# Kernel optimization log

Measured on AMD Instinct MI355X. Metric: run time of the kernel, lower is better.

The kernel has to match this reference:

```python
import jax, jax.numpy as jnp
import numpy as np

B, S, D = 2, 2048, 2048
H, KVH, HD = 16, 4, 128
E, TOPK, FF = 8, 2, 4096
EPS = 1e-6
THETA = 1000000.0


def setup_inputs() -> dict:
    key = jax.random.key(0)
    ks = jax.random.split(key, 12)
    s = 0.02
    return {
        'hidden_states': jax.random.normal(ks[0], (B, S, D), jnp.float32),
        'attention_mask': jnp.ones((B, S), dtype=bool),
        'wq': jax.random.normal(ks[1], (D, H * HD), jnp.float32) * s,
        'wk': jax.random.normal(ks[2], (D, KVH * HD), jnp.float32) * s,
        'wv': jax.random.normal(ks[3], (D, KVH * HD), jnp.float32) * s,
        'wo': jax.random.normal(ks[4], (H * HD, D), jnp.float32) * s,
        'ln1_w': jnp.ones((D,), jnp.float32),
        'ln2_w': jnp.ones((D,), jnp.float32),
        'gate_w': jax.random.normal(ks[5], (D, E), jnp.float32) * s,
        'w_gate': jax.random.normal(ks[6], (E, D, FF), jnp.float32) * s,
        'w_up': jax.random.normal(ks[7], (E, D, FF), jnp.float32) * s,
        'w_down': jax.random.normal(ks[8], (E, FF, D), jnp.float32) * s,
    }


def rms_norm(x, w):
    xf = x.astype(jnp.float32)
    var = jnp.mean(jnp.square(xf), axis=-1, keepdims=True)
    return w * (xf * jax.lax.rsqrt(var + EPS)).astype(x.dtype)


def rotate_half(x):
    x1, x2 = x[..., : x.shape[-1] // 2], x[..., x.shape[-1] // 2 :]
    return jnp.concatenate((-x2, x1), axis=-1)


def attention(x, mask, wq, wk, wv, wo):
    q = (x @ wq).reshape(B, S, H, HD)
    k = (x @ wk).reshape(B, S, KVH, HD)
    v = (x @ wv).reshape(B, S, KVH, HD)
    # RoPE (fp32 freqs, as in MixtralRotaryEmbedding)
    inv_freq = 1.0 / (THETA ** (jnp.arange(0, HD, 2, dtype=jnp.float32) / HD))
    freqs = jnp.arange(S, dtype=jnp.float32)[:, None] * inv_freq[None, :]  # [S, HD/2]
    emb = jnp.concatenate([freqs, freqs], axis=-1)  # [S, HD]
    cos = jnp.cos(emb)[None, :, None, :]  # [1,S,1,HD]
    sin = jnp.sin(emb)[None, :, None, :]
    q = q * cos + rotate_half(q) * sin
    k = k * cos + rotate_half(k) * sin
    # GQA: repeat kv heads
    k = jnp.repeat(k, H // KVH, axis=2)
    v = jnp.repeat(v, H // KVH, axis=2)
    # faithful to source: keep-mask is triu(ones, k=1) (strictly-above-diagonal)
    causal = jnp.triu(jnp.ones((S, S), dtype=bool), k=1)
    combined = mask[:, None, None, :] & causal[None, None, :, :]  # [B,1,S,S]
    neg = jnp.finfo(jnp.float32).min
    bias = jnp.where(combined, 0.0, neg).astype(jnp.float32)
    scores = jnp.einsum('bqhd,bkhd->bhqk', q, k) * (HD ** -0.5) + bias
    attn = jax.nn.softmax(scores, axis=-1)
    out = jnp.einsum('bhqk,bkhd->bqhd', attn, v).reshape(B, S, H * HD)
    return out @ wo


def moe(x, gate_w, w_gate, w_up, w_down):
    # x: [T, D]
    T = x.shape[0]
    logits = x.astype(jnp.float32) @ gate_w  # fp32 router, [T, E]
    rw = jax.nn.softmax(logits, axis=-1)
    top_w, top_i = jax.lax.top_k(rw, TOPK)
    top_w = top_w / jnp.sum(top_w, axis=-1, keepdims=True)
    w_full = jnp.zeros((T, E), jnp.float32).at[jnp.arange(T)[:, None], top_i].set(top_w)
    out = jnp.zeros_like(x)
    for e in range(E):  # small fixed expert loop
        h = jax.nn.silu(x @ w_gate[e]) * (x @ w_up[e])
        out = out + w_full[:, e, None] * (h @ w_down[e])
    return out


def reference(hidden_states, attention_mask, wq, wk, wv, wo, ln1_w, ln2_w, gate_w, w_gate, w_up, w_down):
    residual = hidden_states
    h = rms_norm(hidden_states, ln1_w)
    h = residual + attention(h, attention_mask, wq, wk, wv, wo)
    residual = h
    h = rms_norm(h, ln2_w)
    m = moe(h.reshape(-1, D), gate_w, w_gate, w_up, w_down).reshape(B, S, D)
    return residual + m
```

## Files before the change

kernel.cpp:

```cpp
#include <hip/hip_runtime.h>
#include <cstdint>
#include <cstddef>


typedef unsigned short u16;
typedef __attribute__((ext_vector_type(8))) short short8;
typedef __attribute__((ext_vector_type(8))) _Float16 half8;
typedef __attribute__((ext_vector_type(8))) __bf16 bf16x8;
typedef __attribute__((ext_vector_type(4))) float f32x4;
typedef __attribute__((ext_vector_type(4))) u16 us4;
typedef __attribute__((ext_vector_type(4))) unsigned int u32x4;

__device__ __forceinline__ u16 f2bf(float f) {
  unsigned u = __builtin_bit_cast(unsigned, f);
  u += 0x7fffu + ((u >> 16) & 1u);
  return (u16)(u >> 16);
}
__device__ __forceinline__ void splitf16(float x, float scale, u16 &hi, u16 &lo) {
  float xs = x * scale;
  _Float16 h = (_Float16)xs;
  hi = __builtin_bit_cast(u16, h);
  _Float16 l = (_Float16)(xs - (float)h);
  lo = __builtin_bit_cast(u16, l);
}
__device__ __forceinline__ f32x4 mma_bf(short8 a, short8 b, f32x4 c) {
  return __builtin_amdgcn_mfma_f32_16x16x32_bf16(
      __builtin_bit_cast(bf16x8, a), __builtin_bit_cast(bf16x8, b), c, 0, 0, 0);
}
__device__ __forceinline__ f32x4 mma_h(short8 a, short8 b, f32x4 c) {
  return __builtin_amdgcn_mfma_f32_16x16x32_f16(
      __builtin_bit_cast(half8, a), __builtin_bit_cast(half8, b), c, 0, 0, 0);
}
__device__ __forceinline__ void gl16(const u16 *g, u16 *l) {
  __builtin_amdgcn_global_load_lds(
      (const __attribute__((address_space(1))) unsigned *)g,
      (__attribute__((address_space(3))) unsigned *)l, 16, 0, 0);
}

template <int OM>
__global__ __launch_bounds__(256) void k_trans(
    const float *__restrict__ src, u16 *__restrict__ d0, u16 *__restrict__ d1,
    int ld_src, int ld_dst, long long zhi, long long zlo, int zmod,
    long long dstz, int inter, float scale) {
  int z = blockIdx.z;
  src += (long long)(z / zmod) * zhi + (long long)(z % zmod) * zlo;
  d0 += (long long)z * dstz;
  if constexpr (OM == 1) d1 += (long long)z * dstz;
  int r0 = blockIdx.y * 64, c0 = blockIdx.x * 64;
  __shared__ float t[64][65];
  int tx = threadIdx.x;
  int rr = tx >> 4, cc = (tx & 15) * 4;
#pragma unroll
  for (int i = 0; i < 4; i++) {
    float4 v = *(const float4 *)(src + (size_t)(r0 + rr + i * 16) * ld_src + c0 + cc);
    t[rr + i * 16][cc] = v.x; t[rr + i * 16][cc + 1] = v.y;
    t[rr + i * 16][cc + 2] = v.z; t[rr + i * 16][cc + 3] = v.w;
  }
  __syncthreads();
#pragma unroll
  for (int i = 0; i < 4; i++) {
    int c = rr + i * 16;
    int f = c0 + c;
    int drow = (inter < 0) ? f : (((f >> 5) << 6) + (f & 31) + (inter << 5));
    size_t bo = (size_t)drow * ld_dst + r0 + cc;
    if constexpr (OM == 0) {
      us4 o;
#pragma unroll
      for (int j = 0; j < 4; j++) o[j] = f2bf(t[cc + j][c]);
      *(us4 *)(d0 + bo) = o;
    } else {
      us4 oh, ol;
#pragma unroll
      for (int j = 0; j < 4; j++) {
        u16 a, b; splitf16(t[cc + j][c], scale, a, b);
        oh[j] = a; ol[j] = b;
      }
      *(us4 *)(d0 + bo) = oh;
      *(us4 *)(d1 + bo) = ol;
    }
  }
}

__global__ __launch_bounds__(256) void k_rms(
    const float *__restrict__ x, const float *__restrict__ w,
    u16 *__restrict__ oh, u16 *__restrict__ ol, float scale16) {
  int row = blockIdx.x, tid = threadIdx.x;
  const float *xr = x + (size_t)row * 2048;
  float4 v0 = *(const float4 *)(xr + tid * 8);
  float4 v1 = *(const float4 *)(xr + tid * 8 + 4);
  float ss = v0.x * v0.x + v0.y * v0.y + v0.z * v0.z + v0.w * v0.w +
             v1.x * v1.x + v1.y * v1.y + v1.z * v1.z + v1.w * v1.w;
  __shared__ float red[256];
  red[tid] = ss;
  __syncthreads();
  for (int s = 128; s > 0; s >>= 1) {
    if (tid < s) red[tid] += red[tid + s];
    __syncthreads();
  }
  float sc = rsqrtf(red[0] * (1.0f / 2048.0f) + 1e-6f);
  float4 w0 = *(const float4 *)(w + tid * 8);
  float4 w1 = *(const float4 *)(w + tid * 8 + 4);
  float o[8] = {v0.x * sc * w0.x, v0.y * sc * w0.y, v0.z * sc * w0.z, v0.w * sc * w0.w,
                v1.x * sc * w1.x, v1.y * sc * w1.y, v1.z * sc * w1.z, v1.w * sc * w1.w};
  size_t bo = (size_t)row * 2048 + tid * 8;
  if (ol) {
    us4 h0, h1, l0, l1;
#pragma unroll
    for (int j = 0; j < 4; j++) {
      u16 a, b;
      splitf16(o[j], scale16, a, b); h0[j] = a; l0[j] = b;
      splitf16(o[j + 4], scale16, a, b); h1[j] = a; l1[j] = b;
    }
    *(us4 *)(oh + bo) = h0; *(us4 *)(oh + bo + 4) = h1;
    *(us4 *)(ol + bo) = l0; *(us4 *)(ol + bo + 4) = l1;
  } else {
    us4 a, b;
#pragma unroll
    for (int j = 0; j < 4; j++) { a[j] = f2bf(o[j]); b[j] = f2bf(o[j + 4]); }
    *(us4 *)(oh + bo) = a; *(us4 *)(oh + bo + 4) = b;
  }
}

__global__ void k_cs(float2 *__restrict__ cs) {
  int idx = blockIdx.x * 256 + threadIdx.x;
  int s = idx >> 6, i = idx & 63;
  double inv = exp2(-(double)i * (19.931568569324174 / 64.0));
  double ang = (double)s * inv;
  cs[idx] = make_float2((float)cos(ang), (float)sin(ang));
}

__global__ __launch_bounds__(256) void k_rope(
    const float *__restrict__ qkv, const float2 *__restrict__ cs,
    u16 *__restrict__ qh, u16 *__restrict__ ql,
    u16 *__restrict__ kh, u16 *__restrict__ kl) {
  int t = blockIdx.x, tid = threadIdx.x;
  int s = t & 2047;
  const float *bp = qkv + (size_t)t * 3072;
  for (int p = tid; p < 1024; p += 256) {
    int hh = p >> 6, i = p & 63;
    float2 c = cs[s * 64 + i];
    float x1 = bp[hh * 128 + i], x2 = bp[hh * 128 + 64 + i];
    float o1 = x1 * c.x - x2 * c.y, o2 = x2 * c.x + x1 * c.y;
    size_t b1 = (size_t)t * 2048 + hh * 128 + i;
    u16 a, b;
    splitf16(o1, 16.f, a, b); qh[b1] = a; ql[b1] = b;
    splitf16(o2, 16.f, a, b); qh[b1 + 64] = a; ql[b1 + 64] = b;
  }
  {
    int hh = tid >> 6, i = tid & 63;
    float2 c = cs[s * 64 + i];
    float x1 = bp[2048 + hh * 128 + i], x2 = bp[2048 + hh * 128 + 64 + i];
    float o1 = x1 * c.x - x2 * c.y, o2 = x2 * c.x + x1 * c.y;
    size_t b1 = (size_t)t * 512 + hh * 128 + i;
    u16 a, b;
    splitf16(o1, 16.f, a, b); kh[b1] = a; kl[b1] = b;
    splitf16(o2, 16.f, a, b); kh[b1 + 64] = a; kl[b1 + 64] = b;
  }
}

__global__ __launch_bounds__(256) void k_attn(
    const u16 *__restrict__ qh, const u16 *__restrict__ ql,
    const u16 *__restrict__ kh, const u16 *__restrict__ kl,
    const u16 *__restrict__ vh, const u16 *__restrict__ vl,
    u16 *__restrict__ oh, u16 *__restrict__ ol) {
  const int qt = blockIdx.x, kvh = blockIdx.y, b = blockIdx.z;
  const int q0 = qt * 16;
  const int tid = threadIdx.x, wid = tid >> 6, lane = tid & 63;
  const int h = kvh * 4 + wid;
  const int lr = lane & 15, g = lane >> 4, lk = g * 8;
  const float SC = 0.08838834764831845f * 1.44269504088896341f / 256.0f;

  __shared__ alignas(16) u16 KT[2][2][4096];
  __shared__ alignas(16) u16 VT[2][2][4096];
  __shared__ alignas(16) u16 Pb[4][2][512];

  short8 qfh[4], qfl[4];
  {
    size_t qo = (size_t)(b * 2048 + q0 + lr) * 2048 + h * 128 + lk;
#pragma unroll
    for (int c = 0; c < 4; c++) {
      qfh[c] = *(const short8 *)(qh + qo + c * 32);
      qfl[c] = *(const short8 *)(ql + qo + c * 32);
    }
  }
  f32x4 accO[8] = {};
  float m_r[4], l_r[4];
#pragma unroll
  for (int r = 0; r < 4; r++) { m_r[r] = -3.0e38f; l_r[r] = 0.f; }

  const int kv_start = (q0 == 2032) ? 0 : (((q0 + 1) >> 5) << 5);
  const int nIter = (2048 - kv_start) >> 5;

  const u16 *khp = kh + (size_t)(b * 2048) * 512 + kvh * 128;
  const u16 *klp = kl + (size_t)(b * 2048) * 512 + kvh * 128;
  const u16 *vhp = vh + ((size_t)(b * 4 + kvh) * 128) * 2048;
  const u16 *vlp = vl + ((size_t)(b * 4 + kvh) * 128) * 2048;

  auto stage = [&](int bf, int kv0) {
#pragma unroll
    for (int j = 0; j < 2; j++) {
      const int c0 = wid * 128 + j * 64;
      const int cc = c0 + lane;
      const int krow = cc >> 4, kcol = (cc & 15) ^ (krow & 7);
      const size_t kg = (size_t)(kv0 + krow) * 512 + kcol * 8;
      gl16(khp + kg, &KT[bf][0][c0 * 8]);
      gl16(klp + kg, &KT[bf][1][c0 * 8]);
      const int vd = cc >> 2, vi = (cc & 3) ^ (vd & 3);
      const size_t vg = (size_t)vd * 2048 + kv0 + vi * 8;
      gl16(vhp + vg, &VT[bf][0][c0 * 8]);
      gl16(vlp + vg, &VT[bf][1][c0 * 8]);
    }
  };

  stage(0, kv_start);
  __syncthreads();
  int buf = 0;
  for (int it = 0; it < nIter; it++) {
    const int kv0 = kv_start + (it << 5);
    if (it + 1 < nIter) stage(buf ^ 1, kv0 + 32);
    f32x4 s0 = {}, s1 = {};
    {
      const u16 *KhL = KT[buf][0], *KlL = KT[buf][1];
#pragma unroll
      for (int c = 0; c < 4; c++) {
        const int idx0 = lr * 128 + (((c * 4 + g) ^ (lr & 7)) << 3);
        const int idx1 = idx0 + 2048;
        short8 k0h = *(const short8 *)(KhL + idx0);
        short8 k0l = *(const short8 *)(KlL + idx0);
        short8 k1h = *(const short8 *)(KhL + idx1);
        short8 k1l = *(const short8 *)(KlL + idx1);
        s0 = mma_h(qfh[c], k0h, s0); s0 = mma_h(qfh[c], k0l, s0); s0 = mma_h(qfl[c], k0h, s0);
        s1 = mma_h(qfh[c], k1h, s1); s1 = mma_h(qfh[c], k1l, s1); s1 = mma_h(qfl[c], k1h, s1);
      }
    }
    const bool msk = (kv0 <= q0 + 15);
    float alpha[4];
#pragma unroll
    for (int r = 0; r < 4; r++) {
      float v0 = s0[r] * SC, v1 = s1[r] * SC;
      if (msk) {
        int rowq = q0 + g * 4 + r;
        if (kv0 + lr <= rowq) v0 = -3.0e38f;
        if (kv0 + 16 + lr <= rowq) v1 = -3.0e38f;
      }
      float mx = fmaxf(v0, v1);
#pragma unroll
      for (int o = 1; o < 16; o <<= 1) mx = fmaxf(mx, __shfl_xor(mx, o));
      float mn = fmaxf(m_r[r], mx);
      float p0 = exp2f(v0 - mn), p1 = exp2f(v1 - mn);
      float sum = p0 + p1;
#pragma unroll
      for (int o = 1; o < 16; o <<= 1) sum += __shfl_xor(sum, o);
      alpha[r] = exp2f(m_r[r] - mn);
      l_r[r] = l_r[r] * alpha[r] + sum;
      m_r[r] = mn;
      const int prow = g * 4 + r;
      const int sc0 = lr | (((0 ^ g) & 3) << 3) + 0;
      (void)sc0;
      {
        int c0l = lr, c1l = 16 + lr;
        int p0i = prow * 32 + ((c0l & 7) | ((((c0l >> 3) ^ g) & 3) << 3));
        int p1i = prow * 32 + ((c1l & 7) | ((((c1l >> 3) ^ g) & 3) << 3));
        u16 x, y;
        splitf16(p0, 16.f, x, y); Pb[wid][0][p0i] = x; Pb[wid][1][p0i] = y;
        splitf16(p1, 16.f, x, y); Pb[wid][0][p1i] = x; Pb[wid][1][p1i] = y;
      }
    }
#pragma unroll
    for (int nt = 0; nt < 8; nt++) {
      f32x4 t = accO[nt];
      t[0] *= alpha[0]; t[1] *= alpha[1]; t[2] *= alpha[2]; t[3] *= alpha[3];
      accO[nt] = t;
    }
    asm volatile("s_waitcnt lgkmcnt(0)" ::: "memory");
    const int pidx = lr * 32 + (((g ^ (lr >> 2)) & 3) << 3);
    short8 pfh = *(const short8 *)(&Pb[wid][0][pidx]);
    short8 pfl = *(const short8 *)(&Pb[wid][1][pidx]);
    {
      const u16 *VhL = VT[buf][0], *VlL = VT[buf][1];
#pragma unroll
      for (int nt = 0; nt < 8; nt++) {
        const int d = nt * 16 + lr;
        const int vidx = d * 32 + (((g ^ (d & 3)) & 3) << 3);
        short8 wfh = *(const short8 *)(VhL + vidx);
        short8 wfl = *(const short8 *)(VlL + vidx);
        f32x4 t = accO[nt];
        t = mma_h(pfh, wfh, t); t = mma_h(pfh, wfl, t); t = mma_h(pfl, wfh, t);
        accO[nt] = t;
      }
    }
    __syncthreads();
    buf ^= 1;
  }
  float inv[4];
#pragma unroll
  for (int r = 0; r < 4; r++) inv[r] = 1.0f / (l_r[r] * 256.0f);
#pragma unroll
  for (int nt = 0; nt < 8; nt++)
#pragma unroll
    for (int r = 0; r < 4; r++) {
      float v = accO[nt][r] * inv[r];
      size_t idx = (size_t)(b * 2048 + q0 + g * 4 + r) * 2048 + h * 128 + nt * 16 + lr;
      u16 x, y; splitf16(v, 16.f, x, y);
      oh[idx] = x; ol[idx] = y;
    }
}

template <int MODE>
__global__ __launch_bounds__(256) void k_gemm(
    const u16 *__restrict__ Ah, const u16 *__restrict__ Al,
    const u16 *__restrict__ Bh, const u16 *__restrict__ Bl,
    int M, int N, int K, int lda, int ldb, int ldc, float descale,
    float *__restrict__ outf, const float *__restrict__ resid,
    u16 *__restrict__ outh,
    const int *__restrict__ offs, const int *__restrict__ counts,
    const int *__restrict__ row_token, const float *__restrict__ row_w) {
  constexpr bool SPLIT = (MODE <= 1);
  const int tid = threadIdx.x;
  const int wid = tid >> 6, lane = tid & 63;
  const int wr = wid >> 1, wc = wid & 1;
  const int l15 = lane & 15, l4 = lane >> 4;
  const int n0 = blockIdx.x * 128, m0 = blockIdx.y * 128;
  int seg = 0, cnt = M;
  if constexpr (MODE >= 2) {
    int e = blockIdx.z;
    seg = offs[e]; cnt = counts[e];
    if (m0 >= cnt) return;
    Bh += (size_t)e * (size_t)N * (size_t)ldb;
  }
  __shared__ alignas(16) u16 AsH[4096], BsH[4096];
  __shared__ alignas(16) u16 AsL[SPLIT ? 4096 : 8], BsL[SPLIT ? 4096 : 8];
  const int r16 = lane >> 2, c8 = (lane & 3) << 3;
  int a0 = m0 + wid * 16 + r16, a1 = a0 + 64;
  if constexpr (MODE >= 2) {
    if (a0 > cnt - 1) a0 = cnt - 1;
    if (a1 > cnt - 1) a1 = cnt - 1;
  }
  const u16 *pa0 = Ah + (size_t)(seg + a0) * lda + c8;
  const u16 *pa1 = Ah + (size_t)(seg + a1) * lda + c8;
  const int b0 = n0 + wid * 16 + r16, b1 = b0 + 64;
  const u16 *pb0 = Bh + (size_t)b0 * ldb + c8;
  const u16 *pb1 = Bh + (size_t)b1 * ldb + c8;
  const u16 *qa0 = nullptr, *qa1 = nullptr, *qb0 = nullptr, *qb1 = nullptr;
  if constexpr (SPLIT) {
    qa0 = Al + (size_t)a0 * lda + c8;
    qa1 = Al + (size_t)a1 * lda + c8;
    qb0 = Bl + (size_t)b0 * ldb + c8;
    qb1 = Bl + (size_t)b1 * ldb + c8;
  }
  u16 *sa0 = AsH + wid * 512, *sa1 = AsH + 2048 + wid * 512;
  u16 *sb0 = BsH + wid * 512, *sb1 = BsH + 2048 + wid * 512;
  f32x4 acc[4][4] = {};
  const int fa = (wr * 64 + l15) * 32 + (l4 << 3);
  const int fb = (wc * 64 + l15) * 32 + (l4 << 3);
  for (int k0 = 0; k0 < K; k0 += 32) {
    gl16(pa0 + k0, sa0); gl16(pa1 + k0, sa1);
    gl16(pb0 + k0, sb0); gl16(pb1 + k0, sb1);
    if constexpr (SPLIT) {
      gl16(qa0 + k0, AsL + wid * 512); gl16(qa1 + k0, AsL + 2048 + wid * 512);
      gl16(qb0 + k0, BsL + wid * 512); gl16(qb1 + k0, BsL + 2048 + wid * 512);
    }
    __syncthreads();
    short8 ah[4], bh[4];
#pragma unroll
    for (int i = 0; i < 4; i++) ah[i] = *(const short8 *)(AsH + fa + i * 512);
#pragma unroll
    for (int i = 0; i < 4; i++) bh[i] = *(const short8 *)(BsH + fb + i * 512);
    if constexpr (SPLIT) {
      short8 al[4], bl[4];
#pragma unroll
      for (int i = 0; i < 4; i++) al[i] = *(const short8 *)(AsL + fa + i * 512);
#pragma unroll
      for (int i = 0; i < 4; i++) bl[i] = *(const short8 *)(BsL + fb + i * 512);
#pragma unroll
      for (int mi = 0; mi < 4; mi++)
#pragma unroll
        for (int ni = 0; ni < 4; ni++) {
          f32x4 c = acc[mi][ni];
          c = mma_h(ah[mi], bh[ni], c);
          c = mma_h(ah[mi], bl[ni], c);
          c = mma_h(al[mi], bh[ni], c);
          acc[mi][ni] = c;
        }
    } else {
#pragma unroll
      for (int mi = 0; mi < 4; mi++)
#pragma unroll
        for (int ni = 0; ni < 4; ni++)
          acc[mi][ni] = mma_bf(ah[mi], bh[ni], acc[mi][ni]);
    }
    __syncthreads();
  }
  if constexpr (MODE == 0 || MODE == 1) {
#pragma unroll
    for (int mi = 0; mi < 4; mi++)
#pragma unroll
      for (int q = 0; q < 4; q++) {
        int row = m0 + wr * 64 + l4 * 4 + mi * 16 + q;
        size_t rb = (size_t)row * ldc;
#pragma unroll
        for (int ni = 0; ni < 4; ni++) {
          int col = n0 + wc * 64 + ni * 16 + l15;
          float v = acc[mi][ni][q] * descale;
          if constexpr (MODE == 1) v += resid[rb + col];
          outf[rb + col] = v;
        }
      }
  } else if constexpr (MODE == 2) {
    int f0 = (n0 + wc * 64) >> 1;
#pragma unroll
    for (int mi = 0; mi < 4; mi++)
#pragma unroll
      for (int q = 0; q < 4; q++) {
        int rl = m0 + wr * 64 + l4 * 4 + mi * 16 + q;
        if (rl < cnt) {
          size_t rb = (size_t)(seg + rl) * ldc;
#pragma unroll
          for (int nt = 0; nt < 2; nt++) {
            float gg = acc[mi][nt][q], u = acc[mi][nt + 2][q];
            float hv = (gg / (1.0f + __expf(-gg))) * u;
            outh[rb + f0 + nt * 16 + l15] = f2bf(hv);
          }
        }
      }
  } else {
#pragma unroll
    for (int mi = 0; mi < 4; mi++)
#pragma unroll
      for (int q = 0; q < 4; q++) {
        int rl = m0 + wr * 64 + l4 * 4 + mi * 16 + q;
        if (rl < cnt) {
          int tok = row_token[seg + rl];
          float w = row_w[seg + rl];
          size_t rb = (size_t)tok * ldc;
#pragma unroll
          for (int ni = 0; ni < 4; ni++)
            atomicAdd(outf + rb + n0 + wc * 64 + ni * 16 + l15,
                      w * acc[mi][ni][q]);
        }
      }
  }
}

__global__ __launch_bounds__(64) void k_router(
    const float *__restrict__ hb, const float *__restrict__ w2,
    const float *__restrict__ gw, int *__restrict__ topi,
    float *__restrict__ topw, int *__restrict__ counts) {
  const int t = blockIdx.x, lane = threadIdx.x;
  const float *xr = hb + (size_t)t * 2048;
  float xs[32];
  float ss = 0.f;
#pragma unroll
  for (int c = 0; c < 8; c++) {
    float4 v = *(const float4 *)(xr + c * 256 + lane * 4);
    xs[c * 4 + 0] = v.x; xs[c * 4 + 1] = v.y; xs[c * 4 + 2] = v.z; xs[c * 4 + 3] = v.w;
    ss += v.x * v.x + v.y * v.y + v.z * v.z + v.w * v.w;
  }
#pragma unroll
  for (int o = 1; o < 64; o <<= 1) ss += __shfl_xor(ss, o);
  const float sc = rsqrtf(ss * (1.0f / 2048.0f) + 1e-6f);
  float acc[8] = {0, 0, 0, 0, 0, 0, 0, 0};
#pragma unroll
  for (int c = 0; c < 8; c++)
#pragma unroll
    for (int j = 0; j < 4; j++) {
      int d = c * 256 + lane * 4 + j;
      float xn = xs[c * 4 + j] * sc * w2[d];
      float4 g0 = *(const float4 *)(gw + (size_t)d * 8);
      float4 g1 = *(const float4 *)(gw + (size_t)d * 8 + 4);
      acc[0] += xn * g0.x; acc[1] += xn * g0.y; acc[2] += xn * g0.z; acc[3] += xn * g0.w;
      acc[4] += xn * g1.x; acc[5] += xn * g1.y; acc[6] += xn * g1.z; acc[7] += xn * g1.w;
    }
#pragma unroll
  for (int e = 0; e < 8; e++) {
    float v = acc[e];
#pragma unroll
    for (int o = 1; o < 64; o <<= 1) v += __shfl_xor(v, o);
    acc[e] = v;
  }
  if (lane == 0) {
    float mx = acc[0];
#pragma unroll
    for (int e = 1; e < 8; e++) mx = fmaxf(mx, acc[e]);
    float p[8];
#pragma unroll
    for (int e = 0; e < 8; e++) p[e] = __expf(acc[e] - mx);
    int e0 = 0;
#pragma unroll
    for (int e = 1; e < 8; e++) if (p[e] > p[e0]) e0 = e;
    int e1 = (e0 == 0) ? 1 : 0;
#pragma unroll
    for (int e = 0; e < 8; e++) if (e != e0 && p[e] > p[e1]) e1 = e;
    float s2 = p[e0] + p[e1];
    topi[t * 2] = e0; topi[t * 2 + 1] = e1;
    topw[t * 2] = p[e0] / s2; topw[t * 2 + 1] = p[e1] / s2;
    atomicAdd(counts + e0, 1);
    atomicAdd(counts + e1, 1);
  }
}

__global__ void k_zero(int *__restrict__ p) {
  if (threadIdx.x < 8) p[threadIdx.x] = 0;
}
__global__ void k_offsets(const int *__restrict__ counts, int *__restrict__ offs,
                          int *__restrict__ cursors) {
  if (threadIdx.x == 0) {
    int o = 0;
    for (int e = 0; e < 8; e++) { offs[e] = o; o += counts[e]; cursors[e] = 0; }
    offs[8] = o;
  }
}
__global__ __launch_bounds__(256) void k_scatter(
    const int *__restrict__ topi, const float *__restrict__ topw,
    const int *__restrict__ offs, int *__restrict__ cursors,
    int *__restrict__ row_token, float *__restrict__ row_w) {
  int t = blockIdx.x * 256 + threadIdx.x;
  if (t >= 4096) return;
#pragma unroll
  for (int s = 0; s < 2; s++) {
    int e = topi[t * 2 + s];
    int pos = offs[e] + atomicAdd(cursors + e, 1);
    row_token[pos] = t;
    row_w[pos] = topw[t * 2 + s];
  }
}
__global__ __launch_bounds__(256) void k_gather(
    const u16 *__restrict__ h2, const int *__restrict__ row_token,
    u16 *__restrict__ xg) {
  int r = blockIdx.x;
  int t = row_token[r];
  ((u32x4 *)(xg + (size_t)r * 2048))[threadIdx.x] =
      ((const u32x4 *)(h2 + (size_t)t * 2048))[threadIdx.x];
}

extern "C" void kernel_launch(void *const *d_in, const int *in_sizes, int n_in,
                              void *d_out, int out_size, void *d_ws,
                              size_t ws_size, hipStream_t stream) {
  const float *hidden = (const float *)d_in[0];
  const float *wq = (const float *)d_in[2];
  const float *wk = (const float *)d_in[3];
  const float *wv = (const float *)d_in[4];
  const float *wo = (const float *)d_in[5];
  const float *ln1 = (const float *)d_in[6];
  const float *ln2 = (const float *)d_in[7];
  const float *gw = (const float *)d_in[8];
  const float *wg = (const float *)d_in[9];
  const float *wu = (const float *)d_in[10];
  const float *wd = (const float *)d_in[11];
  float *out = (float *)d_out;

  char *base = (char *)d_ws;
  size_t off = 0;
  auto alloc = [&](size_t bytes) -> char * {
    char *p = base + off;
    off += (bytes + 255) & ~(size_t)255;
    return p;
  };
  u16 *wqkvTh = (u16 *)alloc((size_t)3072 * 2048 * 2);
  u16 *wqkvTl = (u16 *)alloc((size_t)3072 * 2048 * 2);
  u16 *woTh = (u16 *)alloc((size_t)2048 * 2048 * 2);
  u16 *woTl = (u16 *)alloc((size_t)2048 * 2048 * 2);
  u16 *wguT = (u16 *)alloc((size_t)8 * 8192 * 2048 * 2);
  u16 *wdT = (u16 *)alloc((size_t)8 * 2048 * 4096 * 2);
  u16 *h1h = (u16 *)alloc((size_t)4096 * 2048 * 2);
  u16 *h1l = (u16 *)alloc((size_t)4096 * 2048 * 2);
  float *qkv = (float *)alloc((size_t)4096 * 3072 * 4);
  u16 *qbh = (u16 *)alloc((size_t)4096 * 2048 * 2);
  u16 *qbl = (u16 *)alloc((size_t)4096 * 2048 * 2);
  u16 *kbh = (u16 *)alloc((size_t)4096 * 512 * 2);
  u16 *kbl = (u16 *)alloc((size_t)4096 * 512 * 2);
  u16 *vth = (u16 *)alloc((size_t)8 * 128 * 2048 * 2);
  u16 *vtl = (u16 *)alloc((size_t)8 * 128 * 2048 * 2);
  float2 *cs = (float2 *)alloc((size_t)2048 * 64 * 8);
  u16 *aoh = (u16 *)alloc((size_t)4096 * 2048 * 2);
  u16 *aol = (u16 *)alloc((size_t)4096 * 2048 * 2);
  u16 *h2 = (u16 *)alloc((size_t)4096 * 2048 * 2);
  int *topi = (int *)alloc(4096 * 2 * 4);
  float *topwt = (float *)alloc(4096 * 2 * 4);
  int *counts = (int *)alloc(64 * 4);
  int *offs = (int *)alloc(64 * 4);
  int *cursors = (int *)alloc(64 * 4);
  int *row_token = (int *)alloc(8192 * 4);
  float *row_w = (float *)alloc(8192 * 4);
  u16 *xg = (u16 *)alloc((size_t)8192 * 2048 * 2);
  u16 *Hb = (u16 *)alloc((size_t)8192 * 4096 * 2);
  if (off > ws_size) return;

  dim3 T256(256), T64(64);
  k_cs<<<dim3(512), T256, 0, stream>>>(cs);
  k_trans<1><<<dim3(32, 32, 1), T256, 0, stream>>>(wq, wqkvTh, wqkvTl, 2048, 2048, 0, 0, 1, 0, -1, 256.f);
  k_trans<1><<<dim3(8, 32, 1), T256, 0, stream>>>(wk, wqkvTh + (size_t)2048 * 2048, wqkvTl + (size_t)2048 * 2048, 512, 2048, 0, 0, 1, 0, -1, 256.f);
  k_trans<1><<<dim3(8, 32, 1), T256, 0, stream>>>(wv, wqkvTh + (size_t)2560 * 2048, wqkvTl + (size_t)2560 * 2048, 512, 2048, 0, 0, 1, 0, -1, 256.f);
  k_trans<1><<<dim3(32, 32, 1), T256, 0, stream>>>(wo, woTh, woTl, 2048, 2048, 0, 0, 1, 0, -1, 256.f);
  k_trans<0><<<dim3(64, 32, 8), T256, 0, stream>>>(wg, wguT, nullptr, 4096, 2048, (long long)2048 * 4096, 0, 1, (long long)8192 * 2048, 0, 1.f);
  k_trans<0><<<dim3(64, 32, 8), T256, 0, stream>>>(wu, wguT, nullptr, 4096, 2048, (long long)2048 * 4096, 0, 1, (long long)8192 * 2048, 1, 1.f);
  k_trans<0><<<dim3(32, 64, 8), T256, 0, stream>>>(wd, wdT, nullptr, 2048, 4096, (long long)4096 * 2048, 0, 1, (long long)2048 * 4096, -1, 1.f);
  k_rms<<<dim3(4096), T256, 0, stream>>>(hidden, ln1, h1h, h1l, 16.f);
  k_gemm<0><<<dim3(24, 32, 1), T256, 0, stream>>>(
      h1h, h1l, wqkvTh, wqkvTl, 4096, 3072, 2048, 2048, 2048, 3072,
      1.f / 4096.f, qkv, nullptr, nullptr, nullptr, nullptr, nullptr, nullptr);
  k_rope<<<dim3(4096), T256, 0, stream>>>(qkv, cs, qbh, qbl, kbh, kbl);
  k_trans<1><<<dim3(2, 32, 8), T256, 0, stream>>>(qkv + 2560, vth, vtl, 3072, 2048, (long long)2048 * 3072, 128, 4, (long long)128 * 2048, -1, 16.f);
  k_attn<<<dim3(128, 4, 2), T256, 0, stream>>>(qbh, qbl, kbh, kbl, vth, vtl, aoh, aol);
  k_gemm<1><<<dim3(16, 32, 1), T256, 0, stream>>>(
      aoh, aol, woTh, woTl, 4096, 2048, 2048, 2048, 2048, 2048,
      1.f / 4096.f, out, hidden, nullptr, nullptr, nullptr, nullptr, nullptr);
  k_rms<<<dim3(4096), T256, 0, stream>>>(out, ln2, h2, nullptr, 1.f);
  k_zero<<<dim3(1), T64, 0, stream>>>(counts);
  k_router<<<dim3(4096), T64, 0, stream>>>(out, ln2, gw, topi, topwt, counts);
  k_offsets<<<dim3(1), dim3(1), 0, stream>>>(counts, offs, cursors);
  k_scatter<<<dim3(16), T256, 0, stream>>>(topi, topwt, offs, cursors, row_token, row_w);
  k_gather<<<dim3(8192), T256, 0, stream>>>(h2, row_token, xg);
  k_gemm<2><<<dim3(64, 32, 8), T256, 0, stream>>>(
      xg, nullptr, wguT, nullptr, 4096, 8192, 2048, 2048, 2048, 4096, 1.f,
      nullptr, nullptr, Hb, offs, counts, nullptr, nullptr);
  k_gemm<3><<<dim3(16, 32, 8), T256, 0, stream>>>(
      Hb, nullptr, wdT, nullptr, 4096, 2048, 4096, 4096, 4096, 2048, 1.f,
      out, nullptr, nullptr, offs, counts, row_token, row_w);
  (void)in_sizes; (void)n_in; (void)out_size;
}
```

Measured before the change: 1.770 ms.

## Add pipelined 256x256 bf16 expert GEMM kernel for MoE layers

Splits the MoE expert GEMMs out into a new k_gemm8 kernel with 512 threads, 256x256 output tiles, a 4-stage LDS ring buffer with two tiles of prefetch, XOR-swizzled LDS layout, and s_setprio around MFMA bursts. The old 128x128 kernel keeps only the split-fp16 dense path. This targets LDS/global-load stalls and barrier overhead in the dominant expert GEMMs. The larger tiles waste more work on partial expert segments and reduce the number of blocks, which can lower occupancy.

```diff
diff --git a/kernel.cpp b/kernel.cpp
--- a/kernel.cpp
+++ b/kernel.cpp
@@ -255,8 +255,6 @@
       l_r[r] = l_r[r] * alpha[r] + sum;
       m_r[r] = mn;
       const int prow = g * 4 + r;
-      const int sc0 = lr | (((0 ^ g) & 3) << 3) + 0;
-      (void)sc0;
       {
         int c0l = lr, c1l = 16 + lr;
         int p0i = prow * 32 + ((c0l & 7) | ((((c0l >> 3) ^ g) & 3) << 3));
@@ -311,43 +309,25 @@
     const u16 *__restrict__ Ah, const u16 *__restrict__ Al,
     const u16 *__restrict__ Bh, const u16 *__restrict__ Bl,
     int M, int N, int K, int lda, int ldb, int ldc, float descale,
-    float *__restrict__ outf, const float *__restrict__ resid,
-    u16 *__restrict__ outh,
-    const int *__restrict__ offs, const int *__restrict__ counts,
-    const int *__restrict__ row_token, const float *__restrict__ row_w) {
-  constexpr bool SPLIT = (MODE <= 1);
+    float *__restrict__ outf, const float *__restrict__ resid) {
   const int tid = threadIdx.x;
   const int wid = tid >> 6, lane = tid & 63;
   const int wr = wid >> 1, wc = wid & 1;
   const int l15 = lane & 15, l4 = lane >> 4;
   const int n0 = blockIdx.x * 128, m0 = blockIdx.y * 128;
-  int seg = 0, cnt = M;
-  if constexpr (MODE >= 2) {
-    int e = blockIdx.z;
-    seg = offs[e]; cnt = counts[e];
-    if (m0 >= cnt) return;
-    Bh += (size_t)e * (size_t)N * (size_t)ldb;
-  }
   __shared__ alignas(16) u16 AsH[4096], BsH[4096];
-  __shared__ alignas(16) u16 AsL[SPLIT ? 4096 : 8], BsL[SPLIT ? 4096 : 8];
+  __shared__ alignas(16) u16 AsL[4096], BsL[4096];
   const int r16 = lane >> 2, c8 = (lane & 3) << 3;
   int a0 = m0 + wid * 16 + r16, a1 = a0 + 64;
-  if constexpr (MODE >= 2) {
-    if (a0 > cnt - 1) a0 = cnt - 1;
-    if (a1 > cnt - 1) a1 = cnt - 1;
-  }
-  const u16 *pa0 = Ah + (size_t)(seg + a0) * lda + c8;
-  const u16 *pa1 = Ah + (size_t)(seg + a1) * lda + c8;
+  const u16 *pa0 = Ah + (size_t)a0 * lda + c8;
+  const u16 *pa1 = Ah + (size_t)a1 * lda + c8;
   const int b0 = n0 + wid * 16 + r16, b1 = b0 + 64;
   const u16 *pb0 = Bh + (size_t)b0 * ldb + c8;
   const u16 *pb1 = Bh + (size_t)b1 * ldb + c8;
-  const u16 *qa0 = nullptr, *qa1 = nullptr, *qb0 = nullptr, *qb1 = nullptr;
-  if constexpr (SPLIT) {
-    qa0 = Al + (size_t)a0 * lda + c8;
-    qa1 = Al + (size_t)a1 * lda + c8;
-    qb0 = Bl + (size_t)b0 * ldb + c8;
-    qb1 = Bl + (size_t)b1 * ldb + c8;
-  }
+  const u16 *qa0 = Al + (size_t)a0 * lda + c8;
+  const u16 *qa1 = Al + (size_t)a1 * lda + c8;
+  const u16 *qb0 = Bl + (size_t)b0 * ldb + c8;
+  const u16 *qb1 = Bl + (size_t)b1 * ldb + c8;
   u16 *sa0 = AsH + wid * 512, *sa1 = AsH + 2048 + wid * 512;
   u16 *sb0 = BsH + wid * 512, *sb1 = BsH + 2048 + wid * 512;
   f32x4 acc[4][4] = {};
@@ -356,79 +336,163 @@
   for (int k0 = 0; k0 < K; k0 += 32) {
     gl16(pa0 + k0, sa0); gl16(pa1 + k0, sa1);
     gl16(pb0 + k0, sb0); gl16(pb1 + k0, sb1);
-    if constexpr (SPLIT) {
-      gl16(qa0 + k0, AsL + wid * 512); gl16(qa1 + k0, AsL + 2048 + wid * 512);
-      gl16(qb0 + k0, BsL + wid * 512); gl16(qb1 + k0, BsL + 2048 + wid * 512);
-    }
+    gl16(qa0 + k0, AsL + wid * 512); gl16(qa1 + k0, AsL + 2048 + wid * 512);
+    gl16(qb0 + k0, BsL + wid * 512); gl16(qb1 + k0, BsL + 2048 + wid * 512);
     __syncthreads();
-    short8 ah[4], bh[4];
+    short8 ah[4], bh[4], al[4], bl[4];
 #pragma unroll
     for (int i = 0; i < 4; i++) ah[i] = *(const short8 *)(AsH + fa + i * 512);
 #pragma unroll
     for (int i = 0; i < 4; i++) bh[i] = *(const short8 *)(BsH + fb + i * 512);
-    if constexpr (SPLIT) {
-      short8 al[4], bl[4];
-#pragma unroll
-      for (int i = 0; i < 4; i++) al[i] = *(const short8 *)(AsL + fa + i * 512);
-#pragma unroll
-      for (int i = 0; i < 4; i++) bl[i] = *(const short8 *)(BsL + fb + i * 512);
-#pragma unroll
-      for (int mi = 0; mi < 4; mi++)
-#pragma unroll
-        for (int ni = 0; ni < 4; ni++) {
-          f32x4 c = acc[mi][ni];
-          c = mma_h(ah[mi], bh[ni], c);
-          c = mma_h(ah[mi], bl[ni], c);
-          c = mma_h(al[mi], bh[ni], c);
-          acc[mi][ni] = c;
-        }
-    } else {
-#pragma unroll
-      for (int mi = 0; mi < 4; mi++)
-#pragma unroll
-        for (int ni = 0; ni < 4; ni++)
-          acc[mi][ni] = mma_bf(ah[mi], bh[ni], acc[mi][ni]);
-    }
+#pragma unroll
+    for (int i = 0; i < 4; i++) al[i] = *(const short8 *)(AsL + fa + i * 512);
+#pragma unroll
+    for (int i = 0; i < 4; i++) bl[i] = *(const short8 *)(BsL + fb + i * 512);
+#pragma unroll
+    for (int mi = 0; mi < 4; mi++)
+#pragma unroll
+      for (int ni = 0; ni < 4; ni++) {
+        f32x4 c = acc[mi][ni];
+        c = mma_h(ah[mi], bh[ni], c);
+        c = mma_h(ah[mi], bl[ni], c);
+        c = mma_h(al[mi], bh[ni], c);
+        acc[mi][ni] = c;
+      }
     __syncthreads();
   }
-  if constexpr (MODE == 0 || MODE == 1) {
+#pragma unroll
+  for (int mi = 0; mi < 4; mi++)
+#pragma unroll
+    for (int q = 0; q < 4; q++) {
+      int row = m0 + wr * 64 + l4 * 4 + mi * 16 + q;
+      size_t rb = (size_t)row * ldc;
+#pragma unroll
+      for (int ni = 0; ni < 4; ni++) {
+        int col = n0 + wc * 64 + ni * 16 + l15;
+        float v = acc[mi][ni][q] * descale;
+        if constexpr (MODE == 1) v += resid[rb + col];
+        outf[rb + col] = v;
+      }
+    }
+}
+
+template <int MODE>
+__global__ __launch_bounds__(512, 1) void k_gemm8(
+    const u16 *__restrict__ A, const u16 *__restrict__ Ball,
+    int N, int K, int lda, int ldb, int ldc,
+    float *__restrict__ outf, u16 *__restrict__ outh,
+    const int *__restrict__ offs, const int *__restrict__ counts,
+    const int *__restrict__ row_token, const float *__restrict__ row_w) {
+  const int e = blockIdx.z;
+  const int seg = offs[e], cnt = counts[e];
+  const int m0 = blockIdx.y * 256;
+  if (m0 >= cnt) return;
+  const int n0 = blockIdx.x * 256;
+  const u16 *B = Ball + (size_t)e * (size_t)N * (size_t)ldb;
+  const int tid = threadIdx.x, wid = tid >> 6, lane = tid & 63;
+  const int wr = wid >> 2, wc = wid & 3;
+  const int l15 = lane & 15, l4 = lane >> 4;
+
+  __shared__ alignas(16) u16 Ls[4][2][8192];
+
+  const u16 *pA[2], *pB[2];
+#pragma unroll
+  for (int j = 0; j < 2; j++) {
+    int s = (wid * 2 + j) * 64 + lane;
+    int row = s >> 2;
+    int kc = (s & 3) ^ ((row >> 1) & 3);
+    int ra = m0 + row; if (ra > cnt - 1) ra = cnt - 1;
+    pA[j] = A + (size_t)(seg + ra) * lda + kc * 8;
+    pB[j] = B + (size_t)(n0 + row) * ldb + kc * 8;
+  }
+  int offA[8], offB[4];
+#pragma unroll
+  for (int mi = 0; mi < 8; mi++) {
+    int r = wr * 128 + mi * 16 + l15;
+    offA[mi] = (r * 4 + (l4 ^ ((r >> 1) & 3))) << 3;
+  }
+#pragma unroll
+  for (int ni = 0; ni < 4; ni++) {
+    int r = wc * 64 + ni * 16 + l15;
+    offB[ni] = (r * 4 + (l4 ^ ((r >> 1) & 3))) << 3;
+  }
+
+  f32x4 acc[8][4] = {};
+  const int nT = K >> 5;
+  auto stage = [&](int t, int j) {
+    gl16(pA[j] + (t << 5), &Ls[t & 3][0][(wid * 2 + j) << 9]);
+    gl16(pB[j] + (t << 5), &Ls[t & 3][1][(wid * 2 + j) << 9]);
+  };
+  stage(0, 0); stage(0, 1); stage(1, 0); stage(1, 1);
+  asm volatile("s_waitcnt vmcnt(4)" ::: "memory");
+  __builtin_amdgcn_sched_barrier(0);
+  __builtin_amdgcn_s_barrier();
+  __builtin_amdgcn_sched_barrier(0);
+
+  short8 bf[4], af0[4], af1[4];
+  for (int t = 0; t < nT; t++) {
+    const u16 *LA = &Ls[t & 3][0][0], *LB = &Ls[t & 3][1][0];
+#pragma unroll
+    for (int i = 0; i < 4; i++) bf[i] = *(const short8 *)(LB + offB[i]);
+#pragma unroll
+    for (int i = 0; i < 4; i++) af0[i] = *(const short8 *)(LA + offA[i]);
+    if (t + 2 < nT) stage(t + 2, 0);
+    asm volatile("s_waitcnt lgkmcnt(0)" ::: "memory");
+    __builtin_amdgcn_sched_barrier(0);
+    __builtin_amdgcn_s_setprio(1);
 #pragma unroll
     for (int mi = 0; mi < 4; mi++)
 #pragma unroll
+      for (int ni = 0; ni < 4; ni++)
+        acc[mi][ni] = mma_bf(af0[mi], bf[ni], acc[mi][ni]);
+    __builtin_amdgcn_s_setprio(0);
+#pragma unroll
+    for (int i = 0; i < 4; i++) af1[i] = *(const short8 *)(LA + offA[4 + i]);
+    if (t + 2 < nT) stage(t + 2, 1);
+    asm volatile("s_waitcnt lgkmcnt(0)" ::: "memory");
+    __builtin_amdgcn_sched_barrier(0);
+    __builtin_amdgcn_s_setprio(1);
+#pragma unroll
+    for (int mi = 0; mi < 4; mi++)
+#pragma unroll
+      for (int ni = 0; ni < 4; ni++)
+        acc[4 + mi][ni] = mma_bf(af1[mi], bf[ni], acc[4 + mi][ni]);
+    __builtin_amdgcn_s_setprio(0);
+    if (t + 1 < nT) {
+      if (t + 2 < nT) {
+        asm volatile("s_waitcnt vmcnt(4)" ::: "memory");
+      } else {
+        asm volatile("s_waitcnt vmcnt(0)" ::: "memory");
+      }
+      __builtin_amdgcn_sched_barrier(0);
+      __builtin_amdgcn_s_barrier();
+      __builtin_amdgcn_sched_barrier(0);
+    }
+  }
+
+  if constexpr (MODE == 2) {
+    const int f0 = (n0 + wc * 64) >> 1;
+#pragma unroll
+    for (int mi = 0; mi < 8; mi++)
+#pragma unroll
       for (int q = 0; q < 4; q++) {
-        int row = m0 + wr * 64 + l4 * 4 + mi * 16 + q;
-        size_t rb = (size_t)row * ldc;
-#pragma unroll
-        for (int ni = 0; ni < 4; ni++) {
-          int col = n0 + wc * 64 + ni * 16 + l15;
-          float v = acc[mi][ni][q] * descale;
-          if constexpr (MODE == 1) v += resid[rb + col];
-          outf[rb + col] = v;
-        }
-      }
-  } else if constexpr (MODE == 2) {
-    int f0 = (n0 + wc * 64) >> 1;
-#pragma unroll
-    for (int mi = 0; mi < 4; mi++)
-#pragma unroll
-      for (int q = 0; q < 4; q++) {
-        int rl = m0 + wr * 64 + l4 * 4 + mi * 16 + q;
+        int rl = m0 + wr * 128 + mi * 16 + l4 * 4 + q;
         if (rl < cnt) {
           size_t rb = (size_t)(seg + rl) * ldc;
 #pragma unroll
           for (int nt = 0; nt < 2; nt++) {
-            float gg = acc[mi][nt][q], u = acc[mi][nt + 2][q];
-            float hv = (gg / (1.0f + __expf(-gg))) * u;
+            float g = acc[mi][nt][q], u = acc[mi][nt + 2][q];
+            float hv = (g / (1.0f + __expf(-g))) * u;
             outh[rb + f0 + nt * 16 + l15] = f2bf(hv);
           }
         }
       }
   } else {
 #pragma unroll
-    for (int mi = 0; mi < 4; mi++)
+    for (int mi = 0; mi < 8; mi++)
 #pragma unroll
       for (int q = 0; q < 4; q++) {
-        int rl = m0 + wr * 64 + l4 * 4 + mi * 16 + q;
+        int rl = m0 + wr * 128 + mi * 16 + l4 * 4 + q;
         if (rl < cnt) {
           int tok = row_token[seg + rl];
           float w = row_w[seg + rl];
@@ -598,24 +662,24 @@
   k_rms<<<dim3(4096), T256, 0, stream>>>(hidden, ln1, h1h, h1l, 16.f);
   k_gemm<0><<<dim3(24, 32, 1), T256, 0, stream>>>(
       h1h, h1l, wqkvTh, wqkvTl, 4096, 3072, 2048, 2048, 2048, 3072,
-      1.f / 4096.f, qkv, nullptr, nullptr, nullptr, nullptr, nullptr, nullptr);
+      1.f / 4096.f, qkv, nullptr);
   k_rope<<<dim3(4096), T256, 0, stream>>>(qkv, cs, qbh, qbl, kbh, kbl);
   k_trans<1><<<dim3(2, 32, 8), T256, 0, stream>>>(qkv + 2560, vth, vtl, 3072, 2048, (long long)2048 * 3072, 128, 4, (long long)128 * 2048, -1, 16.f);
   k_attn<<<dim3(128, 4, 2), T256, 0, stream>>>(qbh, qbl, kbh, kbl, vth, vtl, aoh, aol);
   k_gemm<1><<<dim3(16, 32, 1), T256, 0, stream>>>(
       aoh, aol, woTh, woTl, 4096, 2048, 2048, 2048, 2048, 2048,
-      1.f / 4096.f, out, hidden, nullptr, nullptr, nullptr, nullptr, nullptr);
+      1.f / 4096.f, out, hidden);
   k_rms<<<dim3(4096), T256, 0, stream>>>(out, ln2, h2, nullptr, 1.f);
   k_zero<<<dim3(1), T64, 0, stream>>>(counts);
   k_router<<<dim3(4096), T64, 0, stream>>>(out, ln2, gw, topi, topwt, counts);
   k_offsets<<<dim3(1), dim3(1), 0, stream>>>(counts, offs, cursors);
   k_scatter<<<dim3(16), T256, 0, stream>>>(topi, topwt, offs, cursors, row_token, row_w);
   k_gather<<<dim3(8192), T256, 0, stream>>>(h2, row_token, xg);
-  k_gemm<2><<<dim3(64, 32, 8), T256, 0, stream>>>(
-      xg, nullptr, wguT, nullptr, 4096, 8192, 2048, 2048, 2048, 4096, 1.f,
-      nullptr, nullptr, Hb, offs, counts, nullptr, nullptr);
-  k_gemm<3><<<dim3(16, 32, 8), T256, 0, stream>>>(
-      Hb, nullptr, wdT, nullptr, 4096, 2048, 4096, 4096, 4096, 2048, 1.f,
-      out, nullptr, nullptr, offs, counts, row_token, row_w);
+  k_gemm8<2><<<dim3(32, 16, 8), dim3(512), 0, stream>>>(
+      xg, wguT, 8192, 2048, 2048, 2048, 4096,
+      nullptr, Hb, offs, counts, nullptr, nullptr);
+  k_gemm8<3><<<dim3(8, 16, 8), dim3(512), 0, stream>>>(
+      Hb, wdT, 2048, 4096, 4096, 4096, 2048,
+      out, nullptr, offs, counts, row_token, row_w);
   (void)in_sizes; (void)n_in; (void)out_size;
 }
```

Measured after the change: 1.646 ms. -7.0%, faster.
